# Performance work log

Measured on AMD Instinct MI355X. Metric: run time of the kernel, lower is better.

## Reference

```python
import jax, jax.numpy as jnp
import numpy as np

B, S, D, H = 2, 2048, 1024, 16
HD = D // H
FF = 4 * D
EPS = 1e-5


def _ln(x, g, b):
    mu = jnp.mean(x, axis=-1, keepdims=True)
    var = jnp.var(x, axis=-1, keepdims=True)
    return (x - mu) * jax.lax.rsqrt(var + EPS) * g + b


def setup_inputs() -> dict:
    key = jax.random.key(0)
    ks = jax.random.split(key, 8)
    std = 0.02
    inp = {
        'x': jax.random.normal(ks[0], (B, S, D), jnp.float32),
        'mask': jnp.ones((B, S), jnp.int32),
        'Wq': jax.random.normal(ks[1], (D, D), jnp.float32) * std,
        'bq': jnp.zeros((D,), jnp.float32),
        'Wk': jax.random.normal(ks[2], (D, D), jnp.float32) * std,
        'bk': jnp.zeros((D,), jnp.float32),
        'Wv': jax.random.normal(ks[3], (D, D), jnp.float32) * std,
        'bv': jnp.zeros((D,), jnp.float32),
        'Wo': jax.random.normal(ks[4], (D, D), jnp.float32) * std,
        'bo': jnp.zeros((D,), jnp.float32),
        'W1': jax.random.normal(ks[5], (D, FF), jnp.float32) * std,
        'b1': jnp.zeros((FF,), jnp.float32),
        'W2': jax.random.normal(ks[6], (FF, D), jnp.float32) * std,
        'b2': jnp.zeros((D,), jnp.float32),
        'g1': jnp.ones((D,), jnp.float32),
        'be1': jnp.zeros((D,), jnp.float32),
        'g2': jnp.ones((D,), jnp.float32),
        'be2': jnp.zeros((D,), jnp.float32),
    }
    return inp


def reference(x, mask, Wq, bq, Wk, bk, Wv, bv, Wo, bo, W1, b1, W2, b2, g1, be1, g2, be2):
    # multi-head attention (dropout in eval mode => identity)
    q = (x @ Wq + bq).reshape(B, S, H, HD).transpose(0, 2, 1, 3)  # [B,H,S,HD]
    k = (x @ Wk + bk).reshape(B, S, H, HD).transpose(0, 2, 1, 3)
    v = (x @ Wv + bv).reshape(B, S, H, HD).transpose(0, 2, 1, 3)
    scores = jnp.einsum('bhqd,bhkd->bhqk', q, k) / jnp.sqrt(jnp.float32(HD))
    m = mask[:, None, None, :]  # [B,1,1,S] broadcast over queries
    scores = jnp.where(m == 0, jnp.float32(-1e9), scores)
    attn = jax.nn.softmax(scores, axis=-1)
    ao = jnp.einsum('bhqk,bhkd->bhqd', attn, v).transpose(0, 2, 1, 3).reshape(B, S, D)
    attn_out = ao @ Wo + bo
    x1 = _ln(x + attn_out, g1, be1)
    ffn = jax.nn.relu(x1 @ W1 + b1) @ W2 + b2
    return _ln(x1 + ffn, g2, be2)
```

## Files before the change

kernel.cpp:

```cpp
#include <hip/hip_runtime.h>
#include <stdint.h>
#include <stddef.h>

#define B_ 2
#define S_ 2048
#define D_ 1024
#define H_ 16
#define HD_ 64
#define FF_ 4096

typedef unsigned short u16;
typedef __attribute__((ext_vector_type(8))) short bf16x8;
typedef __attribute__((ext_vector_type(4))) float f32x4;

__device__ __forceinline__ u16 f2bf(float f) {
  unsigned u = __float_as_uint(f);
  u += 0x7fffu + ((u >> 16) & 1u);
  return (u16)(u >> 16);
}

__device__ __forceinline__ f32x4 mfma16(bf16x8 a, bf16x8 b, f32x4 c) {
  return __builtin_amdgcn_mfma_f32_16x16x32_bf16(a, b, c, 0, 0, 0);
}

__device__ __forceinline__ void gload16(const void* g, void* l) {
  __builtin_amdgcn_global_load_lds(
      (const __attribute__((address_space(1))) void*)g,
      (__attribute__((address_space(3))) void*)l, 16, 0, 0);
}

__device__ __forceinline__ void swizzle_mn(int& mt, int& nt) {
  int gm = gridDim.x;
  if ((gm & 7) == 0) {
    int bid = blockIdx.y * gm + blockIdx.x;
    int mper = gm >> 3;
    int xcd = bid & 7, idx = bid >> 3;
    mt = xcd * mper + (idx % mper);
    nt = idx / mper;
  } else {
    mt = blockIdx.x;
    nt = blockIdx.y;
  }
}

__global__ __launch_bounds__(256) void prep_kernel(
    const float* __restrict__ x, u16* __restrict__ xb,
    const float* __restrict__ W1, u16* __restrict__ w1T,
    const float* __restrict__ W2, u16* __restrict__ w2T,
    const float* __restrict__ Wq, const float* __restrict__ Wk,
    const float* __restrict__ Wv, const float* __restrict__ Wo,
    u16* __restrict__ wTq, u16* __restrict__ wTk,
    u16* __restrict__ wTv, u16* __restrict__ wTo) {
  int bid = blockIdx.x;
  int tid = threadIdx.x;
  if (bid >= 8192 && bid < 12288) {
    int i = (bid - 8192) * 1024 + tid * 4;
    float4 v = *(const float4*)(x + i);
    ushort4 o = { f2bf(v.x), f2bf(v.y), f2bf(v.z), f2bf(v.w) };
    *(ushort4*)(xb + i) = o;
    return;
  }
  const float* W;
  u16* WT;
  int K, N, k0, n0;
  if (bid < 4096) {
    W = W1; WT = w1T; K = 1024; N = 4096;
    k0 = (bid & 31) * 32; n0 = (bid >> 5) * 32;
  } else if (bid < 8192) {
    int b2 = bid - 4096;
    W = W2; WT = w2T; K = 4096; N = 1024;
    k0 = (b2 >> 5) * 32; n0 = (b2 & 31) * 32;
  } else {
    int t = bid - 12288;
    int z = t >> 10, r = t & 1023;
    W = z == 0 ? Wq : (z == 1 ? Wk : (z == 2 ? Wv : Wo));
    WT = z == 0 ? wTq : (z == 1 ? wTk : (z == 2 ? wTv : wTo));
    K = 1024; N = 1024;
    k0 = (r & 31) * 32; n0 = (r >> 5) * 32;
  }
  __shared__ u16 t[32][33];
  int r = tid >> 3;
  int c = (tid & 7) << 2;
  float4 v = *(const float4*)(W + (size_t)(k0 + r) * N + n0 + c);
  t[r][c + 0] = f2bf(v.x); t[r][c + 1] = f2bf(v.y);
  t[r][c + 2] = f2bf(v.z); t[r][c + 3] = f2bf(v.w);
  __syncthreads();
  ushort4 o;
  o.x = t[c + 0][r]; o.y = t[c + 1][r]; o.z = t[c + 2][r]; o.w = t[c + 3][r];
  *(ushort4*)(WT + (size_t)(n0 + r) * K + k0 + c) = o;
}

__global__ __launch_bounds__(256, 4) void gemm_bt_relu(
    const u16* __restrict__ A, const u16* __restrict__ BT,
    const float* __restrict__ bias, u16* __restrict__ outp,
    int M, int N, int K) {
  __shared__ __align__(16) u16 As[128 * 32];
  __shared__ __align__(16) u16 Bs[128 * 32];
  int tid = threadIdx.x;
  int lane = tid & 63;
  int wave = tid >> 6;
  int quad = lane >> 4;
  int l16 = lane & 15;
  int mt, nt;
  swizzle_mn(mt, nt);
  int m0 = mt * 128;
  int n0 = nt * 128;
  int wm = (wave >> 1) * 64;
  int wn = (wave & 1) * 64;

  f32x4 zero = {0.f, 0.f, 0.f, 0.f};
  f32x4 acc[4][4];
#pragma unroll
  for (int i = 0; i < 4; i++)
#pragma unroll
    for (int j = 0; j < 4; j++) acc[i][j] = zero;

  int c0 = tid, c1 = tid + 256;
  const u16* ga0 = A + (size_t)(m0 + (c0 >> 2)) * K + (c0 & 3) * 8;
  const u16* ga1 = A + (size_t)(m0 + (c1 >> 2)) * K + (c1 & 3) * 8;
  const u16* gb0 = BT + (size_t)(n0 + (c0 >> 2)) * K + (c0 & 3) * 8;
  const u16* gb1 = BT + (size_t)(n0 + (c1 >> 2)) * K + (c1 & 3) * 8;

  for (int k0 = 0; k0 < K; k0 += 32) {
    gload16(ga0 + k0, &As[c0 * 8]);
    gload16(ga1 + k0, &As[c1 * 8]);
    gload16(gb0 + k0, &Bs[c0 * 8]);
    gload16(gb1 + k0, &Bs[c1 * 8]);
    __syncthreads();
    bf16x8 af[4], bfr[4];
#pragma unroll
    for (int i = 0; i < 4; i++)
      af[i] = *(const bf16x8*)&As[(wm + i * 16 + l16) * 32 + quad * 8];
#pragma unroll
    for (int j = 0; j < 4; j++)
      bfr[j] = *(const bf16x8*)&Bs[(wn + j * 16 + l16) * 32 + quad * 8];
#pragma unroll
    for (int i = 0; i < 4; i++)
#pragma unroll
      for (int j = 0; j < 4; j++)
        acc[i][j] = mfma16(af[i], bfr[j], acc[i][j]);
    __syncthreads();
  }

#pragma unroll
  for (int j = 0; j < 4; j++) {
    int gcol = n0 + wn + j * 16 + l16;
    float bv = bias[gcol];
#pragma unroll
    for (int i = 0; i < 4; i++) {
#pragma unroll
      for (int r = 0; r < 4; r++) {
        int grow = m0 + wm + i * 16 + quad * 4 + r;
        float val = acc[i][j][r] + bv;
        outp[(size_t)grow * N + gcol] = f2bf(val > 0.f ? val : 0.f);
      }
    }
  }
}

__global__ __launch_bounds__(256, 4) void gemm_bt_sk4(
    const u16* __restrict__ A, const u16* __restrict__ BT,
    const float* __restrict__ bias,
    float* __restrict__ o0, float* __restrict__ o1,
    float* __restrict__ o2, float* __restrict__ o3,
    int M, int N, int K, int Kc) {
  __shared__ __align__(16) u16 As[128 * 32];
  __shared__ __align__(16) u16 Bs[128 * 32];
  int tid = threadIdx.x;
  int lane = tid & 63;
  int wave = tid >> 6;
  int quad = lane >> 4;
  int l16 = lane & 15;
  int mt, nt;
  swizzle_mn(mt, nt);
  int m0 = mt * 128;
  int n0 = nt * 128;
  int z = blockIdx.z;
  int kb = z * Kc;
  int wm = (wave >> 1) * 64;
  int wn = (wave & 1) * 64;

  f32x4 zero = {0.f, 0.f, 0.f, 0.f};
  f32x4 acc[4][4];
#pragma unroll
  for (int i = 0; i < 4; i++)
#pragma unroll
    for (int j = 0; j < 4; j++) acc[i][j] = zero;

  int c0 = tid, c1 = tid + 256;
  const u16* ga0 = A + (size_t)(m0 + (c0 >> 2)) * K + (c0 & 3) * 8 + kb;
  const u16* ga1 = A + (size_t)(m0 + (c1 >> 2)) * K + (c1 & 3) * 8 + kb;
  const u16* gb0 = BT + (size_t)(n0 + (c0 >> 2)) * K + (c0 & 3) * 8 + kb;
  const u16* gb1 = BT + (size_t)(n0 + (c1 >> 2)) * K + (c1 & 3) * 8 + kb;

  for (int k0 = 0; k0 < Kc; k0 += 32) {
    gload16(ga0 + k0, &As[c0 * 8]);
    gload16(ga1 + k0, &As[c1 * 8]);
    gload16(gb0 + k0, &Bs[c0 * 8]);
    gload16(gb1 + k0, &Bs[c1 * 8]);
    __syncthreads();
    bf16x8 af[4], bfr[4];
#pragma unroll
    for (int i = 0; i < 4; i++)
      af[i] = *(const bf16x8*)&As[(wm + i * 16 + l16) * 32 + quad * 8];
#pragma unroll
    for (int j = 0; j < 4; j++)
      bfr[j] = *(const bf16x8*)&Bs[(wn + j * 16 + l16) * 32 + quad * 8];
#pragma unroll
    for (int i = 0; i < 4; i++)
#pragma unroll
      for (int j = 0; j < 4; j++)
        acc[i][j] = mfma16(af[i], bfr[j], acc[i][j]);
    __syncthreads();
  }

  float* outz = z == 0 ? o0 : (z == 1 ? o1 : (z == 2 ? o2 : o3));
  float biasmul = (z == 0) ? 1.f : 0.f;
#pragma unroll
  for (int j = 0; j < 4; j++) {
    int gcol = n0 + wn + j * 16 + l16;
    float bv = bias[gcol] * biasmul;
#pragma unroll
    for (int i = 0; i < 4; i++) {
#pragma unroll
      for (int r = 0; r < 4; r++) {
        int grow = m0 + wm + i * 16 + quad * 4 + r;
        outz[(size_t)grow * N + gcol] = acc[i][j][r] + bv;
      }
    }
  }
}

__global__ __launch_bounds__(256) void gemm_qkv(
    const u16* __restrict__ A, const u16* __restrict__ BT,
    const float* __restrict__ bq, const float* __restrict__ bk,
    const float* __restrict__ bvp,
    u16* __restrict__ qb, u16* __restrict__ kb, u16* __restrict__ vb) {
  const int K = 1024;
  __shared__ __align__(16) u16 As[128 * 32];
  __shared__ __align__(16) u16 Bs[128 * 32];
  int tid = threadIdx.x;
  int lane = tid & 63;
  int wave = tid >> 6;
  int quad = lane >> 4;
  int l16 = lane & 15;
  int mt, nt;
  swizzle_mn(mt, nt);
  int m0 = mt * 128;
  int n0 = nt * 128;
  int wm = (wave >> 1) * 64;
  int wn = (wave & 1) * 64;

  f32x4 zero = {0.f, 0.f, 0.f, 0.f};
  f32x4 acc[4][4];
#pragma unroll
  for (int i = 0; i < 4; i++)
#pragma unroll
    for (int j = 0; j < 4; j++) acc[i][j] = zero;

  int c0 = tid, c1 = tid + 256;
  const u16* ga0 = A + (size_t)(m0 + (c0 >> 2)) * K + (c0 & 3) * 8;
  const u16* ga1 = A + (size_t)(m0 + (c1 >> 2)) * K + (c1 & 3) * 8;
  const u16* gb0 = BT + (size_t)(n0 + (c0 >> 2)) * K + (c0 & 3) * 8;
  const u16* gb1 = BT + (size_t)(n0 + (c1 >> 2)) * K + (c1 & 3) * 8;

  for (int k0 = 0; k0 < K; k0 += 32) {
    gload16(ga0 + k0, &As[c0 * 8]);
    gload16(ga1 + k0, &As[c1 * 8]);
    gload16(gb0 + k0, &Bs[c0 * 8]);
    gload16(gb1 + k0, &Bs[c1 * 8]);
    __syncthreads();
    bf16x8 af[4], bfr[4];
#pragma unroll
    for (int i = 0; i < 4; i++)
      af[i] = *(const bf16x8*)&As[(wm + i * 16 + l16) * 32 + quad * 8];
#pragma unroll
    for (int j = 0; j < 4; j++)
      bfr[j] = *(const bf16x8*)&Bs[(wn + j * 16 + l16) * 32 + quad * 8];
#pragma unroll
    for (int i = 0; i < 4; i++)
#pragma unroll
      for (int j = 0; j < 4; j++)
        acc[i][j] = mfma16(af[i], bfr[j], acc[i][j]);
    __syncthreads();
  }

  int region = n0 >> 10;
  const float* bias = region == 0 ? bq : (region == 1 ? bk : bvp);
  u16* outp = region == 0 ? qb : (region == 1 ? kb : vb);
  float scale = region == 0 ? 0.125f * 1.4426950408889634f : 1.f;

#pragma unroll
  for (int j = 0; j < 4; j++) {
    int gcol = (n0 & 1023) + wn + j * 16 + l16;
    float bv = bias[gcol];
    int h = gcol >> 6, hd = gcol & 63;
#pragma unroll
    for (int i = 0; i < 4; i++) {
#pragma unroll
      for (int r = 0; r < 4; r++) {
        int grow = m0 + wm + i * 16 + quad * 4 + r;
        float val = (acc[i][j][r] + bv) * scale;
        int b = grow >> 11, s = grow & 2047;
        if (region < 2) {
          outp[(((size_t)(b * H_ + h)) * S_ + s) * HD_ + hd] = f2bf(val);
        } else {
          outp[(((size_t)(b * H_ + h)) * HD_ + hd) * S_ + s] = f2bf(val);
        }
      }
    }
  }
}

__global__ __launch_bounds__(256, 2) void attn_kernel(
    const u16* __restrict__ q, const u16* __restrict__ k,
    const u16* __restrict__ vt, const int* __restrict__ mask,
    u16* __restrict__ ao) {
  __shared__ __align__(16) u16 Ks[2][64 * 72];
  __shared__ __align__(16) u16 Vs[2][64 * 72];
  __shared__ __align__(16) u16 Ps[4][32 * 72];
  int tid = threadIdx.x;
  int lane = tid & 63;
  int wave = tid >> 6;
  int quad = lane >> 4;
  int l16 = lane & 15;
  int bh = blockIdx.y;
  int b = bh >> 4;
  int h = bh & 15;
  int qrow0 = blockIdx.x * 128 + wave * 32;

  const u16* qh = q + (size_t)bh * S_ * HD_;
  const u16* kh = k + (size_t)bh * S_ * HD_;
  const u16* vh = vt + (size_t)bh * HD_ * S_;

  bf16x8 qfA0 = *(const bf16x8*)(qh + (size_t)(qrow0 + l16) * HD_ + quad * 8);
  bf16x8 qfA1 = *(const bf16x8*)(qh + (size_t)(qrow0 + l16) * HD_ + 32 + quad * 8);
  bf16x8 qfB0 = *(const bf16x8*)(qh + (size_t)(qrow0 + 16 + l16) * HD_ + quad * 8);
  bf16x8 qfB1 = *(const bf16x8*)(qh + (size_t)(qrow0 + 16 + l16) * HD_ + 32 + quad * 8);

  int sr = tid >> 3, sc = tid & 7;
  const u16* kg0 = kh + sr * HD_ + sc * 8;
  const u16* kg1 = kh + (sr + 32) * HD_ + sc * 8;
  const u16* vg0 = vh + (size_t)sr * S_ + sc * 8;
  const u16* vg1 = vh + (size_t)(sr + 32) * S_ + sc * 8;
  int kr0 = (sr & 1) * 16 + (sr >> 1);
  int ko0 = kr0 * 72 + sc * 8;
  int ko1 = (32 + kr0) * 72 + sc * 8;
  int vo0 = sr * 72 + sc * 8;
  int vo1 = (sr + 32) * 72 + sc * 8;
  const int* mrow = mask + b * S_ + 2 * l16;

  float l_pA[4] = {0.f, 0.f, 0.f, 0.f};
  float l_pB[4] = {0.f, 0.f, 0.f, 0.f};
  f32x4 zero = {0.f, 0.f, 0.f, 0.f};
  f32x4 o_accA[4], o_accB[4];
#pragma unroll
  for (int c = 0; c < 4; c++) { o_accA[c] = zero; o_accB[c] = zero; }

  u16* pw = &Ps[wave][0];

  bf16x8 kv0 = *(const bf16x8*)(kg0);
  bf16x8 kv1 = *(const bf16x8*)(kg1);
  bf16x8 vv0 = *(const bf16x8*)(vg0);
  bf16x8 vv1 = *(const bf16x8*)(vg1);
  *(bf16x8*)&Ks[0][ko0] = kv0;
  *(bf16x8*)&Ks[0][ko1] = kv1;
  *(bf16x8*)&Vs[0][vo0] = vv0;
  *(bf16x8*)&Vs[0][vo1] = vv1;
  kv0 = *(const bf16x8*)(kg0 + (size_t)64 * HD_);
  kv1 = *(const bf16x8*)(kg1 + (size_t)64 * HD_);
  vv0 = *(const bf16x8*)(vg0 + 64);
  vv1 = *(const bf16x8*)(vg1 + 64);

  int cur = 0;
  for (int kt = 0; kt < S_; kt += 64) {
    int2 mk0 = *(const int2*)(mrow + kt);
    int2 mk1 = *(const int2*)(mrow + kt + 32);

    __syncthreads();
    if (kt + 64 < S_) {
      int alt = cur ^ 1;
      *(bf16x8*)&Ks[alt][ko0] = kv0;
      *(bf16x8*)&Ks[alt][ko1] = kv1;
      *(bf16x8*)&Vs[alt][vo0] = vv0;
      *(bf16x8*)&Vs[alt][vo1] = vv1;
      int nk = (kt + 128) & (S_ - 1);
      kv0 = *(const bf16x8*)(kg0 + (size_t)nk * HD_);
      kv1 = *(const bf16x8*)(kg1 + (size_t)nk * HD_);
      vv0 = *(const bf16x8*)(vg0 + nk);
      vv1 = *(const bf16x8*)(vg1 + nk);
    }

    const u16* ksb = &Ks[cur][0];
    const u16* vsb = &Vs[cur][0];
#pragma unroll
    for (int g = 0; g < 2; g++) {
      int2 mk = g == 0 ? mk0 : mk1;
      int rowe = (g * 32 + l16) * 72;
      int rowo = (g * 32 + 16 + l16) * 72;
      bf16x8 e0 = *(const bf16x8*)&ksb[rowe + quad * 8];
      bf16x8 e1 = *(const bf16x8*)&ksb[rowe + 32 + quad * 8];
      bf16x8 o0 = *(const bf16x8*)&ksb[rowo + quad * 8];
      bf16x8 o1 = *(const bf16x8*)&ksb[rowo + 32 + quad * 8];
      f32x4 seA = mfma16(qfA1, e1, mfma16(qfA0, e0, zero));
      f32x4 soA = mfma16(qfA1, o1, mfma16(qfA0, o0, zero));
      f32x4 seB = mfma16(qfB1, e1, mfma16(qfB0, e0, zero));
      f32x4 soB = mfma16(qfB1, o1, mfma16(qfB0, o0, zero));
#pragma unroll
      for (int r = 0; r < 4; r++) {
        float pA0 = mk.x ? exp2f(seA[r]) : 0.f;
        float pA1 = mk.y ? exp2f(soA[r]) : 0.f;
        float pB0 = mk.x ? exp2f(seB[r]) : 0.f;
        float pB1 = mk.y ? exp2f(soB[r]) : 0.f;
        l_pA[r] += pA0 + pA1;
        l_pB[r] += pB0 + pB1;
        unsigned pkA = __builtin_amdgcn_perm(__float_as_uint(pA1),
                                             __float_as_uint(pA0), 0x07060302u);
        unsigned pkB = __builtin_amdgcn_perm(__float_as_uint(pB1),
                                             __float_as_uint(pB0), 0x07060302u);
        *(unsigned*)&pw[(quad * 4 + r) * 72 + g * 32 + 2 * l16] = pkA;
        *(unsigned*)&pw[(16 + quad * 4 + r) * 72 + g * 32 + 2 * l16] = pkB;
      }
    }
    bf16x8 pfA0 = *(const bf16x8*)&pw[l16 * 72 + quad * 8];
    bf16x8 pfA1 = *(const bf16x8*)&pw[l16 * 72 + 32 + quad * 8];
    bf16x8 pfB0 = *(const bf16x8*)&pw[(16 + l16) * 72 + quad * 8];
    bf16x8 pfB1 = *(const bf16x8*)&pw[(16 + l16) * 72 + 32 + quad * 8];
#pragma unroll
    for (int c = 0; c < 4; c++) {
      bf16x8 vf0 = *(const bf16x8*)&vsb[(c * 16 + l16) * 72 + quad * 8];
      bf16x8 vf1 = *(const bf16x8*)&vsb[(c * 16 + l16) * 72 + 32 + quad * 8];
      o_accA[c] = mfma16(pfA1, vf1, mfma16(pfA0, vf0, o_accA[c]));
      o_accB[c] = mfma16(pfB1, vf1, mfma16(pfB0, vf0, o_accB[c]));
    }
    cur ^= 1;
  }

#pragma unroll
  for (int r = 0; r < 4; r++) {
    float sA = l_pA[r], sB = l_pB[r];
#pragma unroll
    for (int off = 1; off < 16; off <<= 1) {
      sA += __shfl_xor(sA, off);
      sB += __shfl_xor(sB, off);
    }
    float invA = 1.f / sA, invB = 1.f / sB;
    int srowA = qrow0 + quad * 4 + r;
    int srowB = qrow0 + 16 + quad * 4 + r;
#pragma unroll
    for (int c = 0; c < 4; c++) {
      ao[((size_t)(b * S_ + srowA)) * D_ + h * HD_ + c * 16 + l16] =
          f2bf(o_accA[c][r] * invA);
      ao[((size_t)(b * S_ + srowB)) * D_ + h * HD_ + c * 16 + l16] =
          f2bf(o_accB[c][r] * invB);
    }
  }
}

__global__ __launch_bounds__(256) void ln_kernel(
    const float* __restrict__ xa, const float* __restrict__ add0,
    const float* __restrict__ add1,
    const float* __restrict__ g, const float* __restrict__ be,
    float* __restrict__ outf, u16* __restrict__ outb) {
  int row = blockIdx.x;
  int tid = threadIdx.x;
  int lane = tid & 63;
  int wv = tid >> 6;
  const float4 a = *(const float4*)(xa + (size_t)row * D_ + tid * 4);
  const float4 c = *(const float4*)(add0 + (size_t)row * D_ + tid * 4);
  const float4 d = *(const float4*)(add1 + (size_t)row * D_ + tid * 4);
  float v0 = a.x + c.x + d.x, v1 = a.y + c.y + d.y;
  float v2 = a.z + c.z + d.z, v3 = a.w + c.w + d.w;
  float s = v0 + v1 + v2 + v3;
  float sq = v0 * v0 + v1 * v1 + v2 * v2 + v3 * v3;
#pragma unroll
  for (int off = 1; off < 64; off <<= 1) {
    s += __shfl_xor(s, off);
    sq += __shfl_xor(sq, off);
  }
  __shared__ float red[8];
  if (lane == 0) { red[wv] = s; red[4 + wv] = sq; }
  __syncthreads();
  s = red[0] + red[1] + red[2] + red[3];
  sq = red[4] + red[5] + red[6] + red[7];
  float mean = s * (1.f / D_);
  float var = sq * (1.f / D_) - mean * mean;
  float rstd = rsqrtf(var + 1e-5f);
  const float4 gv = *(const float4*)(g + tid * 4);
  const float4 bv = *(const float4*)(be + tid * 4);
  float y0 = (v0 - mean) * rstd * gv.x + bv.x;
  float y1 = (v1 - mean) * rstd * gv.y + bv.y;
  float y2 = (v2 - mean) * rstd * gv.z + bv.z;
  float y3 = (v3 - mean) * rstd * gv.w + bv.w;
  float4 o = {y0, y1, y2, y3};
  *(float4*)(outf + (size_t)row * D_ + tid * 4) = o;
  if (outb) {
    ushort4 ob = {f2bf(y0), f2bf(y1), f2bf(y2), f2bf(y3)};
    *(ushort4*)(outb + (size_t)row * D_ + tid * 4) = ob;
  }
}

__global__ __launch_bounds__(256) void ln4_kernel(
    const float* __restrict__ xa,
    const float* __restrict__ a0, const float* __restrict__ a1,
    const float* __restrict__ a2, const float* __restrict__ a3,
    const float* __restrict__ g, const float* __restrict__ be,
    float* __restrict__ outf, u16* __restrict__ outb) {
  int row = blockIdx.x;
  int tid = threadIdx.x;
  int lane = tid & 63;
  int wv = tid >> 6;
  size_t off0 = (size_t)row * D_ + tid * 4;
  const float4 a = *(const float4*)(xa + off0);
  const float4 c0 = *(const float4*)(a0 + off0);
  const float4 c1 = *(const float4*)(a1 + off0);
  const float4 c2 = *(const float4*)(a2 + off0);
  const float4 c3 = *(const float4*)(a3 + off0);
  float v0 = a.x + (c0.x + c1.x) + (c2.x + c3.x);
  float v1 = a.y + (c0.y + c1.y) + (c2.y + c3.y);
  float v2 = a.z + (c0.z + c1.z) + (c2.z + c3.z);
  float v3 = a.w + (c0.w + c1.w) + (c2.w + c3.w);
  float s = v0 + v1 + v2 + v3;
  float sq = v0 * v0 + v1 * v1 + v2 * v2 + v3 * v3;
#pragma unroll
  for (int off = 1; off < 64; off <<= 1) {
    s += __shfl_xor(s, off);
    sq += __shfl_xor(sq, off);
  }
  __shared__ float red[8];
  if (lane == 0) { red[wv] = s; red[4 + wv] = sq; }
  __syncthreads();
  s = red[0] + red[1] + red[2] + red[3];
  sq = red[4] + red[5] + red[6] + red[7];
  float mean = s * (1.f / D_);
  float var = sq * (1.f / D_) - mean * mean;
  float rstd = rsqrtf(var + 1e-5f);
  const float4 gv = *(const float4*)(g + tid * 4);
  const float4 bv = *(const float4*)(be + tid * 4);
  float y0 = (v0 - mean) * rstd * gv.x + bv.x;
  float y1 = (v1 - mean) * rstd * gv.y + bv.y;
  float y2 = (v2 - mean) * rstd * gv.z + bv.z;
  float y3 = (v3 - mean) * rstd * gv.w + bv.w;
  float4 o = {y0, y1, y2, y3};
  *(float4*)(outf + off0) = o;
  if (outb) {
    ushort4 ob = {f2bf(y0), f2bf(y1), f2bf(y2), f2bf(y3)};
    *(ushort4*)(outb + off0) = ob;
  }
}

extern "C" void kernel_launch(void* const* d_in, const int* in_sizes, int n_in,
                              void* d_out, int out_size, void* d_ws, size_t ws_size,
                              hipStream_t stream) {
  const float* x = (const float*)d_in[0];
  const int* mask = (const int*)d_in[1];
  const float* Wq = (const float*)d_in[2];
  const float* bq = (const float*)d_in[3];
  const float* Wk = (const float*)d_in[4];
  const float* bk = (const float*)d_in[5];
  const float* Wv = (const float*)d_in[6];
  const float* bv = (const float*)d_in[7];
  const float* Wo = (const float*)d_in[8];
  const float* bo = (const float*)d_in[9];
  const float* W1 = (const float*)d_in[10];
  const float* b1 = (const float*)d_in[11];
  const float* W2 = (const float*)d_in[12];
  const float* b2 = (const float*)d_in[13];
  const float* g1 = (const float*)d_in[14];
  const float* be1 = (const float*)d_in[15];
  const float* g2 = (const float*)d_in[16];
  const float* be2 = (const float*)d_in[17];

  const size_t MB = 1ull << 20;
  char* ws = (char*)d_ws;
  u16* wTq = (u16*)(ws + 0 * MB);
  u16* wTk = (u16*)(ws + 2 * MB);
  u16* wTv = (u16*)(ws + 4 * MB);
  u16* wTo = (u16*)(ws + 6 * MB);
  u16* w1T = (u16*)(ws + 8 * MB);
  u16* w2T = (u16*)(ws + 16 * MB);
  u16* xb  = (u16*)(ws + 24 * MB);
  u16* qb  = (u16*)(ws + 32 * MB);
  u16* kb  = (u16*)(ws + 40 * MB);
  u16* vb  = (u16*)(ws + 48 * MB);
  u16* ao  = (u16*)(ws + 56 * MB);
  float* p0 = (float*)(ws + 64 * MB);
  float* p1 = (float*)(ws + 80 * MB);
  float* x1f = (float*)(ws + 24 * MB);
  u16*   x1b = (u16*)(ws + 40 * MB);
  u16*   h1  = (u16*)(ws + 48 * MB);
  float* f0 = (float*)(ws + 80 * MB);
  float* f1 = (float*)(ws + 96 * MB);
  float* f2 = (float*)(ws + 112 * MB);
  float* f3 = (float*)(ws + 0 * MB);

  prep_kernel<<<dim3(16384), dim3(256), 0, stream>>>(
      x, xb, W1, w1T, W2, w2T, Wq, Wk, Wv, Wo, wTq, wTk, wTv, wTo);

  gemm_qkv<<<dim3(32, 24), dim3(256), 0, stream>>>(xb, wTq, bq, bk, bv, qb, kb, vb);

  attn_kernel<<<dim3(S_ / 128, B_ * H_), dim3(256), 0, stream>>>(qb, kb, vb, mask, ao);

  gemm_bt_sk4<<<dim3(32, 8, 2), dim3(256), 0, stream>>>(
      ao, wTo, bo, p0, p1, p0, p0, 4096, 1024, 1024, 512);

  ln_kernel<<<dim3(4096), dim3(256), 0, stream>>>(x, p0, p1, g1, be1, x1f, x1b);

  gemm_bt_relu<<<dim3(32, 32), dim3(256), 0, stream>>>(x1b, w1T, b1, h1, 4096, 4096, 1024);

  gemm_bt_sk4<<<dim3(32, 8, 4), dim3(256), 0, stream>>>(
      h1, w2T, b2, f0, f1, f2, f3, 4096, 1024, 4096, 1024);

  ln4_kernel<<<dim3(4096), dim3(256), 0, stream>>>(
      x1f, f0, f1, f2, f3, g2, be2, (float*)d_out, (u16*)nullptr);
}
```

Baseline: 371.1 us.

## Halve attention query tile per wave and remap blocks by XCD

Each wave now processes 16 query rows instead of 32, and each block covers 64 rows, doubling the attention grid and shrinking registers and P shared memory so three blocks can fit per CU. Block indices are remapped so that blocks sharing a head land on the same XCD, improving L2 reuse of K/V. The cost is that each K/V tile loaded to LDS feeds half as many MFMAs, increasing load traffic per flop.

```diff
diff --git a/kernel.cpp b/kernel.cpp
--- a/kernel.cpp
+++ b/kernel.cpp
@@ -312,31 +312,35 @@
   }
 }
 
-__global__ __launch_bounds__(256, 2) void attn_kernel(
+__global__ __launch_bounds__(256, 3) void attn_kernel(
     const u16* __restrict__ q, const u16* __restrict__ k,
     const u16* __restrict__ vt, const int* __restrict__ mask,
     u16* __restrict__ ao) {
   __shared__ __align__(16) u16 Ks[2][64 * 72];
   __shared__ __align__(16) u16 Vs[2][64 * 72];
-  __shared__ __align__(16) u16 Ps[4][32 * 72];
+  __shared__ __align__(16) u16 Ps[4][16 * 72];
   int tid = threadIdx.x;
   int lane = tid & 63;
   int wave = tid >> 6;
   int quad = lane >> 4;
   int l16 = lane & 15;
-  int bh = blockIdx.y;
+
+  int lin = blockIdx.y * gridDim.x + blockIdx.x;
+  int xcd = lin & 7;
+  int t = lin >> 3;
+  int qb = t & 31;
+  int hh = t >> 5;
+  int bh = hh * 8 + xcd;
   int b = bh >> 4;
   int h = bh & 15;
-  int qrow0 = blockIdx.x * 128 + wave * 32;
+  int qrow0 = qb * 64 + wave * 16;
 
   const u16* qh = q + (size_t)bh * S_ * HD_;
   const u16* kh = k + (size_t)bh * S_ * HD_;
   const u16* vh = vt + (size_t)bh * HD_ * S_;
 
-  bf16x8 qfA0 = *(const bf16x8*)(qh + (size_t)(qrow0 + l16) * HD_ + quad * 8);
-  bf16x8 qfA1 = *(const bf16x8*)(qh + (size_t)(qrow0 + l16) * HD_ + 32 + quad * 8);
-  bf16x8 qfB0 = *(const bf16x8*)(qh + (size_t)(qrow0 + 16 + l16) * HD_ + quad * 8);
-  bf16x8 qfB1 = *(const bf16x8*)(qh + (size_t)(qrow0 + 16 + l16) * HD_ + 32 + quad * 8);
+  bf16x8 qf0 = *(const bf16x8*)(qh + (size_t)(qrow0 + l16) * HD_ + quad * 8);
+  bf16x8 qf1 = *(const bf16x8*)(qh + (size_t)(qrow0 + l16) * HD_ + 32 + quad * 8);
 
   int sr = tid >> 3, sc = tid & 7;
   const u16* kg0 = kh + sr * HD_ + sc * 8;
@@ -350,12 +354,11 @@
   int vo1 = (sr + 32) * 72 + sc * 8;
   const int* mrow = mask + b * S_ + 2 * l16;
 
-  float l_pA[4] = {0.f, 0.f, 0.f, 0.f};
-  float l_pB[4] = {0.f, 0.f, 0.f, 0.f};
+  float l_p[4] = {0.f, 0.f, 0.f, 0.f};
   f32x4 zero = {0.f, 0.f, 0.f, 0.f};
-  f32x4 o_accA[4], o_accB[4];
-#pragma unroll
-  for (int c = 0; c < 4; c++) { o_accA[c] = zero; o_accB[c] = zero; }
+  f32x4 o_acc[4];
+#pragma unroll
+  for (int c = 0; c < 4; c++) o_acc[c] = zero;
 
   u16* pw = &Ps[wave][0];
 
@@ -402,57 +405,42 @@
       bf16x8 e1 = *(const bf16x8*)&ksb[rowe + 32 + quad * 8];
       bf16x8 o0 = *(const bf16x8*)&ksb[rowo + quad * 8];
       bf16x8 o1 = *(const bf16x8*)&ksb[rowo + 32 + quad * 8];
-      f32x4 seA = mfma16(qfA1, e1, mfma16(qfA0, e0, zero));
-      f32x4 soA = mfma16(qfA1, o1, mfma16(qfA0, o0, zero));
-      f32x4 seB = mfma16(qfB1, e1, mfma16(qfB0, e0, zero));
-      f32x4 soB = mfma16(qfB1, o1, mfma16(qfB0, o0, zero));
+      f32x4 se = mfma16(qf1, e1, mfma16(qf0, e0, zero));
+      f32x4 so = mfma16(qf1, o1, mfma16(qf0, o0, zero));
 #pragma unroll
       for (int r = 0; r < 4; r++) {
-        float pA0 = mk.x ? exp2f(seA[r]) : 0.f;
-        float pA1 = mk.y ? exp2f(soA[r]) : 0.f;
-        float pB0 = mk.x ? exp2f(seB[r]) : 0.f;
-        float pB1 = mk.y ? exp2f(soB[r]) : 0.f;
-        l_pA[r] += pA0 + pA1;
-        l_pB[r] += pB0 + pB1;
-        unsigned pkA = __builtin_amdgcn_perm(__float_as_uint(pA1),
-                                             __float_as_uint(pA0), 0x07060302u);
-        unsigned pkB = __builtin_amdgcn_perm(__float_as_uint(pB1),
-                                             __float_as_uint(pB0), 0x07060302u);
-        *(unsigned*)&pw[(quad * 4 + r) * 72 + g * 32 + 2 * l16] = pkA;
-        *(unsigned*)&pw[(16 + quad * 4 + r) * 72 + g * 32 + 2 * l16] = pkB;
+        float p0 = mk.x ? exp2f(se[r]) : 0.f;
+        float p1 = mk.y ? exp2f(so[r]) : 0.f;
+        l_p[r] += p0 + p1;
+        unsigned pk = __builtin_amdgcn_perm(__float_as_uint(p1),
+                                            __float_as_uint(p0), 0x07060302u);
+        *(unsigned*)&pw[(quad * 4 + r) * 72 + g * 32 + 2 * l16] = pk;
       }
     }
-    bf16x8 pfA0 = *(const bf16x8*)&pw[l16 * 72 + quad * 8];
-    bf16x8 pfA1 = *(const bf16x8*)&pw[l16 * 72 + 32 + quad * 8];
-    bf16x8 pfB0 = *(const bf16x8*)&pw[(16 + l16) * 72 + quad * 8];
-    bf16x8 pfB1 = *(const bf16x8*)&pw[(16 + l16) * 72 + 32 + quad * 8];
+    bf16x8 pf0 = *(const bf16x8*)&pw[l16 * 72 + quad * 8];
+    bf16x8 pf1 = *(const bf16x8*)&pw[l16 * 72 + 32 + quad * 8];
 #pragma unroll
     for (int c = 0; c < 4; c++) {
       bf16x8 vf0 = *(const bf16x8*)&vsb[(c * 16 + l16) * 72 + quad * 8];
       bf16x8 vf1 = *(const bf16x8*)&vsb[(c * 16 + l16) * 72 + 32 + quad * 8];
-      o_accA[c] = mfma16(pfA1, vf1, mfma16(pfA0, vf0, o_accA[c]));
-      o_accB[c] = mfma16(pfB1, vf1, mfma16(pfB0, vf0, o_accB[c]));
+      o_acc[c] = mfma16(pf1, vf1, mfma16(pf0, vf0, o_acc[c]));
     }
     cur ^= 1;
   }
 
 #pragma unroll
   for (int r = 0; r < 4; r++) {
-    float sA = l_pA[r], sB = l_pB[r];
+    float sA = l_p[r];
 #pragma unroll
     for (int off = 1; off < 16; off <<= 1) {
       sA += __shfl_xor(sA, off);
-      sB += __shfl_xor(sB, off);
-    }
-    float invA = 1.f / sA, invB = 1.f / sB;
-    int srowA = qrow0 + quad * 4 + r;
-    int srowB = qrow0 + 16 + quad * 4 + r;
+    }
+    float invA = 1.f / sA;
+    int srow = qrow0 + quad * 4 + r;
 #pragma unroll
     for (int c = 0; c < 4; c++) {
-      ao[((size_t)(b * S_ + srowA)) * D_ + h * HD_ + c * 16 + l16] =
-          f2bf(o_accA[c][r] * invA);
-      ao[((size_t)(b * S_ + srowB)) * D_ + h * HD_ + c * 16 + l16] =
-          f2bf(o_accB[c][r] * invB);
+      ao[((size_t)(b * S_ + srow)) * D_ + h * HD_ + c * 16 + l16] =
+          f2bf(o_acc[c][r] * invA);
     }
   }
 }
@@ -599,7 +587,7 @@
 
   gemm_qkv<<<dim3(32, 24), dim3(256), 0, stream>>>(xb, wTq, bq, bk, bv, qb, kb, vb);
 
-  attn_kernel<<<dim3(S_ / 128, B_ * H_), dim3(256), 0, stream>>>(qb, kb, vb, mask, ao);
+  attn_kernel<<<dim3(32, 32), dim3(256), 0, stream>>>(qb, kb, vb, mask, ao);
 
   gemm_bt_sk4<<<dim3(32, 8, 2), dim3(256), 0, stream>>>(
       ao, wTo, bo, p0, p1, p0, p0, 4096, 1024, 1024, 512);
```

Result: slower. 380.6 us (+2.5%).

## Load K/V fragments directly from global memory and remap blocks per XCD

Applied to the files above, without the earlier changes.

The attention kernel drops the shared-memory double-buffered K/V staging and its per-iteration __syncthreads. Each wave now loads its K and V^T MFMA fragments straight from global memory, relying on L2 to serve the copies that the four waves share. Block indices are also remapped so that all query tiles of one head land on the same XCD, which should improve L2 reuse of that head's K/V. The trade-off is four times more global/L2 traffic per block and no software prefetch, so load latency is exposed inside the loop.

```diff
diff --git a/kernel.cpp b/kernel.cpp
--- a/kernel.cpp
+++ b/kernel.cpp
@@ -316,18 +316,22 @@
     const u16* __restrict__ q, const u16* __restrict__ k,
     const u16* __restrict__ vt, const int* __restrict__ mask,
     u16* __restrict__ ao) {
-  __shared__ __align__(16) u16 Ks[2][64 * 72];
-  __shared__ __align__(16) u16 Vs[2][64 * 72];
   __shared__ __align__(16) u16 Ps[4][32 * 72];
   int tid = threadIdx.x;
   int lane = tid & 63;
   int wave = tid >> 6;
   int quad = lane >> 4;
   int l16 = lane & 15;
-  int bh = blockIdx.y;
+
+  int lin = blockIdx.y * gridDim.x + blockIdx.x;
+  int xcd = lin & 7;
+  int t = lin >> 3;
+  int qt = t & 15;
+  int hh = t >> 4;
+  int bh = hh * 8 + xcd;
   int b = bh >> 4;
   int h = bh & 15;
-  int qrow0 = blockIdx.x * 128 + wave * 32;
+  int qrow0 = qt * 128 + wave * 32;
 
   const u16* qh = q + (size_t)bh * S_ * HD_;
   const u16* kh = k + (size_t)bh * S_ * HD_;
@@ -338,16 +342,9 @@
   bf16x8 qfB0 = *(const bf16x8*)(qh + (size_t)(qrow0 + 16 + l16) * HD_ + quad * 8);
   bf16x8 qfB1 = *(const bf16x8*)(qh + (size_t)(qrow0 + 16 + l16) * HD_ + 32 + quad * 8);
 
-  int sr = tid >> 3, sc = tid & 7;
-  const u16* kg0 = kh + sr * HD_ + sc * 8;
-  const u16* kg1 = kh + (sr + 32) * HD_ + sc * 8;
-  const u16* vg0 = vh + (size_t)sr * S_ + sc * 8;
-  const u16* vg1 = vh + (size_t)(sr + 32) * S_ + sc * 8;
-  int kr0 = (sr & 1) * 16 + (sr >> 1);
-  int ko0 = kr0 * 72 + sc * 8;
-  int ko1 = (32 + kr0) * 72 + sc * 8;
-  int vo0 = sr * 72 + sc * 8;
-  int vo1 = (sr + 32) * 72 + sc * 8;
+  const u16* ke = kh + (size_t)(2 * l16) * HD_ + quad * 8;
+  const u16* kod = kh + (size_t)(2 * l16 + 1) * HD_ + quad * 8;
+  const u16* vbase = vh + (size_t)l16 * S_ + quad * 8;
   const int* mrow = mask + b * S_ + 2 * l16;
 
   float l_pA[4] = {0.f, 0.f, 0.f, 0.f};
@@ -359,49 +356,37 @@
 
   u16* pw = &Ps[wave][0];
 
-  bf16x8 kv0 = *(const bf16x8*)(kg0);
-  bf16x8 kv1 = *(const bf16x8*)(kg1);
-  bf16x8 vv0 = *(const bf16x8*)(vg0);
-  bf16x8 vv1 = *(const bf16x8*)(vg1);
-  *(bf16x8*)&Ks[0][ko0] = kv0;
-  *(bf16x8*)&Ks[0][ko1] = kv1;
-  *(bf16x8*)&Vs[0][vo0] = vv0;
-  *(bf16x8*)&Vs[0][vo1] = vv1;
-  kv0 = *(const bf16x8*)(kg0 + (size_t)64 * HD_);
-  kv1 = *(const bf16x8*)(kg1 + (size_t)64 * HD_);
-  vv0 = *(const bf16x8*)(vg0 + 64);
-  vv1 = *(const bf16x8*)(vg1 + 64);
-
-  int cur = 0;
   for (int kt = 0; kt < S_; kt += 64) {
     int2 mk0 = *(const int2*)(mrow + kt);
     int2 mk1 = *(const int2*)(mrow + kt + 32);
 
-    __syncthreads();
-    if (kt + 64 < S_) {
-      int alt = cur ^ 1;
-      *(bf16x8*)&Ks[alt][ko0] = kv0;
-      *(bf16x8*)&Ks[alt][ko1] = kv1;
-      *(bf16x8*)&Vs[alt][vo0] = vv0;
-      *(bf16x8*)&Vs[alt][vo1] = vv1;
-      int nk = (kt + 128) & (S_ - 1);
-      kv0 = *(const bf16x8*)(kg0 + (size_t)nk * HD_);
-      kv1 = *(const bf16x8*)(kg1 + (size_t)nk * HD_);
-      vv0 = *(const bf16x8*)(vg0 + nk);
-      vv1 = *(const bf16x8*)(vg1 + nk);
-    }
-
-    const u16* ksb = &Ks[cur][0];
-    const u16* vsb = &Vs[cur][0];
+    const u16* ke0p = ke + (size_t)kt * HD_;
+    const u16* ko0p = kod + (size_t)kt * HD_;
+    const u16* ke1p = ke + (size_t)(kt + 32) * HD_;
+    const u16* ko1p = kod + (size_t)(kt + 32) * HD_;
+    bf16x8 e00 = *(const bf16x8*)(ke0p);
+    bf16x8 e01 = *(const bf16x8*)(ke0p + 32);
+    bf16x8 o00 = *(const bf16x8*)(ko0p);
+    bf16x8 o01 = *(const bf16x8*)(ko0p + 32);
+    bf16x8 e10 = *(const bf16x8*)(ke1p);
+    bf16x8 e11 = *(const bf16x8*)(ke1p + 32);
+    bf16x8 o10 = *(const bf16x8*)(ko1p);
+    bf16x8 o11 = *(const bf16x8*)(ko1p + 32);
+    bf16x8 vf[4][2];
+#pragma unroll
+    for (int c = 0; c < 4; c++) {
+      const u16* vp = vbase + (size_t)(c * 16) * S_ + kt;
+      vf[c][0] = *(const bf16x8*)(vp);
+      vf[c][1] = *(const bf16x8*)(vp + 32);
+    }
+
 #pragma unroll
     for (int g = 0; g < 2; g++) {
       int2 mk = g == 0 ? mk0 : mk1;
-      int rowe = (g * 32 + l16) * 72;
-      int rowo = (g * 32 + 16 + l16) * 72;
-      bf16x8 e0 = *(const bf16x8*)&ksb[rowe + quad * 8];
-      bf16x8 e1 = *(const bf16x8*)&ksb[rowe + 32 + quad * 8];
-      bf16x8 o0 = *(const bf16x8*)&ksb[rowo + quad * 8];
-      bf16x8 o1 = *(const bf16x8*)&ksb[rowo + 32 + quad * 8];
+      bf16x8 e0 = g == 0 ? e00 : e10;
+      bf16x8 e1 = g == 0 ? e01 : e11;
+      bf16x8 o0 = g == 0 ? o00 : o10;
+      bf16x8 o1 = g == 0 ? o01 : o11;
       f32x4 seA = mfma16(qfA1, e1, mfma16(qfA0, e0, zero));
       f32x4 soA = mfma16(qfA1, o1, mfma16(qfA0, o0, zero));
       f32x4 seB = mfma16(qfB1, e1, mfma16(qfB0, e0, zero));
@@ -428,12 +413,9 @@
     bf16x8 pfB1 = *(const bf16x8*)&pw[(16 + l16) * 72 + 32 + quad * 8];
 #pragma unroll
     for (int c = 0; c < 4; c++) {
-      bf16x8 vf0 = *(const bf16x8*)&vsb[(c * 16 + l16) * 72 + quad * 8];
-      bf16x8 vf1 = *(const bf16x8*)&vsb[(c * 16 + l16) * 72 + 32 + quad * 8];
-      o_accA[c] = mfma16(pfA1, vf1, mfma16(pfA0, vf0, o_accA[c]));
-      o_accB[c] = mfma16(pfB1, vf1, mfma16(pfB0, vf0, o_accB[c]));
-    }
-    cur ^= 1;
+      o_accA[c] = mfma16(pfA1, vf[c][1], mfma16(pfA0, vf[c][0], o_accA[c]));
+      o_accB[c] = mfma16(pfB1, vf[c][1], mfma16(pfB0, vf[c][0], o_accB[c]));
+    }
   }
 
 #pragma unroll
@@ -599,7 +581,7 @@
 
   gemm_qkv<<<dim3(32, 24), dim3(256), 0, stream>>>(xb, wTq, bq, bk, bv, qb, kb, vb);
 
-  attn_kernel<<<dim3(S_ / 128, B_ * H_), dim3(256), 0, stream>>>(qb, kb, vb, mask, ao);
+  attn_kernel<<<dim3(16, 32), dim3(256), 0, stream>>>(qb, kb, vb, mask, ao);
 
   gemm_bt_sk4<<<dim3(32, 8, 2), dim3(256), 0, stream>>>(
       ao, wTo, bo, p0, p1, p0, p0, 4096, 1024, 1024, 512);
```

New measurement: 424.9 us. 1.14x slower.

## Split attention over two key halves with combine kernel and XCD-aware block mapping

Applied to the files above, without the earlier changes.

Splits each attention block's key range into two halves, doubling the grid to 1024 blocks. Each block writes unnormalized fp32 partial outputs and row sums, and a new combine kernel sums them and normalizes to bf16. Blocks are remapped so each head stays on one XCD, and K/V staging drops from double to single buffering with an extra barrier, allowing 4 blocks per CU. This targets low occupancy and poor L2 locality, at the cost of an extra kernel, fp32 partial traffic, and lost load/compute overlap. The combine relies on the scores having no running max, matching the original kernel's exp2 without max subtraction.

```diff
diff --git a/kernel.cpp b/kernel.cpp
--- a/kernel.cpp
+++ b/kernel.cpp
@@ -312,22 +312,30 @@
   }
 }
 
-__global__ __launch_bounds__(256, 2) void attn_kernel(
+__global__ __launch_bounds__(256, 4) void attn_kernel(
     const u16* __restrict__ q, const u16* __restrict__ k,
     const u16* __restrict__ vt, const int* __restrict__ mask,
-    u16* __restrict__ ao) {
-  __shared__ __align__(16) u16 Ks[2][64 * 72];
-  __shared__ __align__(16) u16 Vs[2][64 * 72];
+    float* __restrict__ po, float* __restrict__ pl) {
+  __shared__ __align__(16) u16 Ks[64 * 72];
+  __shared__ __align__(16) u16 Vs[64 * 72];
   __shared__ __align__(16) u16 Ps[4][32 * 72];
   int tid = threadIdx.x;
   int lane = tid & 63;
   int wave = tid >> 6;
   int quad = lane >> 4;
   int l16 = lane & 15;
-  int bh = blockIdx.y;
+
+  int lin = blockIdx.y * gridDim.x + blockIdx.x;
+  int xcd = lin & 7;
+  int t = lin >> 3;
+  int qt = t & 15;
+  int half = (t >> 4) & 1;
+  int hh = t >> 5;
+  int bh = hh * 8 + xcd;
   int b = bh >> 4;
   int h = bh & 15;
-  int qrow0 = blockIdx.x * 128 + wave * 32;
+  int qrow0 = qt * 128 + wave * 32;
+  int kb = half * (S_ / 2);
 
   const u16* qh = q + (size_t)bh * S_ * HD_;
   const u16* kh = k + (size_t)bh * S_ * HD_;
@@ -359,40 +367,31 @@
 
   u16* pw = &Ps[wave][0];
 
-  bf16x8 kv0 = *(const bf16x8*)(kg0);
-  bf16x8 kv1 = *(const bf16x8*)(kg1);
-  bf16x8 vv0 = *(const bf16x8*)(vg0);
-  bf16x8 vv1 = *(const bf16x8*)(vg1);
-  *(bf16x8*)&Ks[0][ko0] = kv0;
-  *(bf16x8*)&Ks[0][ko1] = kv1;
-  *(bf16x8*)&Vs[0][vo0] = vv0;
-  *(bf16x8*)&Vs[0][vo1] = vv1;
-  kv0 = *(const bf16x8*)(kg0 + (size_t)64 * HD_);
-  kv1 = *(const bf16x8*)(kg1 + (size_t)64 * HD_);
-  vv0 = *(const bf16x8*)(vg0 + 64);
-  vv1 = *(const bf16x8*)(vg1 + 64);
-
-  int cur = 0;
-  for (int kt = 0; kt < S_; kt += 64) {
+  bf16x8 kv0 = *(const bf16x8*)(kg0 + (size_t)kb * HD_);
+  bf16x8 kv1 = *(const bf16x8*)(kg1 + (size_t)kb * HD_);
+  bf16x8 vv0 = *(const bf16x8*)(vg0 + kb);
+  bf16x8 vv1 = *(const bf16x8*)(vg1 + kb);
+
+  for (int kt = kb; kt < kb + S_ / 2; kt += 64) {
     int2 mk0 = *(const int2*)(mrow + kt);
     int2 mk1 = *(const int2*)(mrow + kt + 32);
 
     __syncthreads();
-    if (kt + 64 < S_) {
-      int alt = cur ^ 1;
-      *(bf16x8*)&Ks[alt][ko0] = kv0;
-      *(bf16x8*)&Ks[alt][ko1] = kv1;
-      *(bf16x8*)&Vs[alt][vo0] = vv0;
-      *(bf16x8*)&Vs[alt][vo1] = vv1;
-      int nk = (kt + 128) & (S_ - 1);
+    *(bf16x8*)&Ks[ko0] = kv0;
+    *(bf16x8*)&Ks[ko1] = kv1;
+    *(bf16x8*)&Vs[vo0] = vv0;
+    *(bf16x8*)&Vs[vo1] = vv1;
+    if (kt + 64 < kb + S_ / 2) {
+      int nk = kt + 64;
       kv0 = *(const bf16x8*)(kg0 + (size_t)nk * HD_);
       kv1 = *(const bf16x8*)(kg1 + (size_t)nk * HD_);
       vv0 = *(const bf16x8*)(vg0 + nk);
       vv1 = *(const bf16x8*)(vg1 + nk);
     }
-
-    const u16* ksb = &Ks[cur][0];
-    const u16* vsb = &Vs[cur][0];
+    __syncthreads();
+
+    const u16* ksb = &Ks[0];
+    const u16* vsb = &Vs[0];
 #pragma unroll
     for (int g = 0; g < 2; g++) {
       int2 mk = g == 0 ? mk0 : mk1;
@@ -433,9 +432,10 @@
       o_accA[c] = mfma16(pfA1, vf1, mfma16(pfA0, vf0, o_accA[c]));
       o_accB[c] = mfma16(pfB1, vf1, mfma16(pfB0, vf0, o_accB[c]));
     }
-    cur ^= 1;
-  }
-
+  }
+
+  float* poh = po + (size_t)half * ((size_t)B_ * S_ * D_);
+  float* plh = pl + (size_t)half * ((size_t)B_ * H_ * S_);
 #pragma unroll
   for (int r = 0; r < 4; r++) {
     float sA = l_pA[r], sB = l_pB[r];
@@ -444,17 +444,39 @@
       sA += __shfl_xor(sA, off);
       sB += __shfl_xor(sB, off);
     }
-    float invA = 1.f / sA, invB = 1.f / sB;
     int srowA = qrow0 + quad * 4 + r;
     int srowB = qrow0 + 16 + quad * 4 + r;
+    if (l16 == 0) {
+      plh[(size_t)bh * S_ + srowA] = sA;
+      plh[(size_t)bh * S_ + srowB] = sB;
+    }
 #pragma unroll
     for (int c = 0; c < 4; c++) {
-      ao[((size_t)(b * S_ + srowA)) * D_ + h * HD_ + c * 16 + l16] =
-          f2bf(o_accA[c][r] * invA);
-      ao[((size_t)(b * S_ + srowB)) * D_ + h * HD_ + c * 16 + l16] =
-          f2bf(o_accB[c][r] * invB);
-    }
-  }
+      poh[((size_t)(b * S_ + srowA)) * D_ + h * HD_ + c * 16 + l16] =
+          o_accA[c][r];
+      poh[((size_t)(b * S_ + srowB)) * D_ + h * HD_ + c * 16 + l16] =
+          o_accB[c][r];
+    }
+  }
+}
+
+__global__ __launch_bounds__(256) void attn_combine(
+    const float* __restrict__ po, const float* __restrict__ pl,
+    u16* __restrict__ ao) {
+  int row = blockIdx.x;
+  int tid = threadIdx.x;
+  int b = row >> 11, s = row & 2047;
+  int h = tid >> 4;
+  const size_t NPO = (size_t)B_ * S_ * D_;
+  size_t off = (size_t)row * D_ + tid * 4;
+  float4 o0 = *(const float4*)(po + off);
+  float4 o1 = *(const float4*)(po + NPO + off);
+  size_t li = ((size_t)(b * H_ + h)) * S_ + s;
+  float l0 = pl[li], l1 = pl[(size_t)B_ * H_ * S_ + li];
+  float inv = 1.f / (l0 + l1);
+  ushort4 o = { f2bf((o0.x + o1.x) * inv), f2bf((o0.y + o1.y) * inv),
+                f2bf((o0.z + o1.z) * inv), f2bf((o0.w + o1.w) * inv) };
+  *(ushort4*)(ao + off) = o;
 }
 
 __global__ __launch_bounds__(256) void ln_kernel(
@@ -584,6 +606,8 @@
   u16* kb  = (u16*)(ws + 40 * MB);
   u16* vb  = (u16*)(ws + 48 * MB);
   u16* ao  = (u16*)(ws + 56 * MB);
+  float* po = (float*)(ws + 64 * MB);
+  float* pl = (float*)(ws + 96 * MB);
   float* p0 = (float*)(ws + 64 * MB);
   float* p1 = (float*)(ws + 80 * MB);
   float* x1f = (float*)(ws + 24 * MB);
@@ -599,7 +623,9 @@
 
   gemm_qkv<<<dim3(32, 24), dim3(256), 0, stream>>>(xb, wTq, bq, bk, bv, qb, kb, vb);
 
-  attn_kernel<<<dim3(S_ / 128, B_ * H_), dim3(256), 0, stream>>>(qb, kb, vb, mask, ao);
+  attn_kernel<<<dim3(32, 32), dim3(256), 0, stream>>>(qb, kb, vb, mask, po, pl);
+
+  attn_combine<<<dim3(4096), dim3(256), 0, stream>>>(po, pl, ao);
 
   gemm_bt_sk4<<<dim3(32, 8, 2), dim3(256), 0, stream>>>(
       ao, wTo, bo, p0, p1, p0, p0, 4096, 1024, 1024, 512);
```

Result: slower. 382.5 us (+3.0%).
